# Optimization experiments

Measured on AMD Instinct MI355X. Metric: run time of the kernel, lower is better.

Reference implementation:

```python
import jax, jax.numpy as jnp
import numpy as np

EPS = 1e-5

def _ln(x, g, b):
    m = jnp.mean(x, axis=-1, keepdims=True)
    v = jnp.mean((x - m) ** 2, axis=-1, keepdims=True)
    return (x - m) / jnp.sqrt(v + EPS) * g + b

B, SX, SY = 2, 2048, 2048
XD, YD, P, H, MULT = 1024, 1024, 64, 16, 4

def setup_inputs() -> dict:
    key = jax.random.key(0)
    ks = jax.random.split(key, 20)
    s = lambda fan: 1.0 / np.sqrt(fan)
    return {
        "x": jax.random.normal(ks[0], (B, SX, XD), jnp.float32),
        "y": jax.random.normal(ks[1], (B, SY, YD), jnp.float32),
        "gx_gamma": jnp.ones((XD,), jnp.float32),
        "gx_beta": jnp.zeros((XD,), jnp.float32),
        "gy_gamma": jnp.ones((YD,), jnp.float32),
        "gy_beta": jnp.zeros((YD,), jnp.float32),
        "Wq": jax.random.uniform(ks[2], (H, XD, P), jnp.float32, -s(XD), s(XD)),
        "bq": jax.random.uniform(ks[3], (H, P), jnp.float32, -s(XD), s(XD)),
        "Wk": jax.random.uniform(ks[4], (H, YD, P), jnp.float32, -s(YD), s(YD)),
        "bk": jax.random.uniform(ks[5], (H, P), jnp.float32, -s(YD), s(YD)),
        "Wv": jax.random.uniform(ks[6], (H, YD, P), jnp.float32, -s(YD), s(YD)),
        "bv": jax.random.uniform(ks[7], (H, P), jnp.float32, -s(YD), s(YD)),
        "Wo": jax.random.uniform(ks[8], (H * P, XD), jnp.float32, -s(H * P), s(H * P)),
        "bo": jax.random.uniform(ks[9], (XD,), jnp.float32, -s(H * P), s(H * P)),
        "gd_gamma": jnp.ones((XD,), jnp.float32),
        "gd_beta": jnp.zeros((XD,), jnp.float32),
        "W1": jax.random.uniform(ks[10], (XD, MULT * XD), jnp.float32, -s(XD), s(XD)),
        "b1": jax.random.uniform(ks[11], (MULT * XD,), jnp.float32, -s(XD), s(XD)),
        "W2": jax.random.uniform(ks[12], (MULT * XD, XD), jnp.float32, -s(MULT * XD), s(MULT * XD)),
        "b2": jax.random.uniform(ks[13], (XD,), jnp.float32, -s(MULT * XD), s(MULT * XD)),
        "mask": 1,
    }

def reference(x, y, gx_gamma, gx_beta, gy_gamma, gy_beta, Wq, bq, Wk, bk, Wv, bv,
              Wo, bo, gd_gamma, gd_beta, W1, b1, W2, b2, mask):
    xn = _ln(x, gx_gamma, gx_beta)
    yn = _ln(y, gy_gamma, gy_beta)
    # batched per-head projections: [B,S,D] x [H,D,P] -> [B,H,S,P]
    q = jnp.einsum('bsd,hdp->bhsp', xn, Wq) + bq[None, :, None, :]
    k = jnp.einsum('btd,hdp->bhtp', yn, Wk) + bk[None, :, None, :]
    v = jnp.einsum('btd,hdp->bhtp', yn, Wv) + bv[None, :, None, :]
    scores = jnp.einsum('bhsp,bhtp->bhst', q, k) * (1.0 / jnp.sqrt(jnp.float32(P)))
    attn = jax.nn.softmax(scores, axis=-1)
    if mask:
        # post-softmax strictly-upper-triangular mask (torch.triu diagonal=1)
        tri = jnp.triu(jnp.ones((SX, SY), attn.dtype), k=1)
        attn = attn * tri
    o = jnp.einsum('bhst,bhtp->bhsp', attn, v)          # [B,H,S,P]
    o = o.transpose(0, 2, 1, 3).reshape(B, SX, H * P)    # concat heads
    x2 = x + o @ Wo + bo
    h = jax.nn.gelu(_ln(x2, gd_gamma, gd_beta) @ W1 + b1, approximate=False)
    return x2 + h @ W2 + b2
```

## Files before the change

kernel.cpp:

```cpp
#include <hip/hip_runtime.h>
#include <hip/hip_bf16.h>
#include <math.h>

typedef __bf16 bf16_t;
typedef __bf16 bf16x8 __attribute__((ext_vector_type(8)));
typedef __bf16 bf16x4 __attribute__((ext_vector_type(4)));
typedef float f32x4 __attribute__((ext_vector_type(4)));

#define QSCALE 0.18033688011112042f

static __device__ __forceinline__ f32x4 mfma16(bf16x8 a, bf16x8 b, f32x4 c) {
  return __builtin_amdgcn_mfma_f32_16x16x32_bf16(a, b, c, 0, 0, 0);
}

static __device__ __forceinline__ float exp2_fast(float x) {
  float r;
  asm("v_exp_f32 %0, %1" : "=v"(r) : "v"(x));
  return r;
}

static __device__ __forceinline__ float gelu_f(float x) {
  const float u = x * (0.7978845608028654f + 0.03567740813636141f * x * x);
  const float a = fminf(u * 2.885390081777927f, 126.0f);
  const float e = exp2_fast(a);
  float r;
  asm("v_rcp_f32 %0, %1" : "=v"(r) : "v"(e + 1.0f));
  return x * e * r;
}

typedef __attribute__((address_space(1))) const void as1_void;
typedef __attribute__((address_space(3))) void as3_void;
static __device__ __forceinline__ void gload16(const void* g, void* s) {
  __builtin_amdgcn_global_load_lds((as1_void*)g, (as3_void*)s, 16, 0, 0);
}

static __device__ __forceinline__ long hmi(int row, int col) {
  return ((((long)(row >> 11) * 16 + (col >> 6)) * 2048) + (row & 2047)) * 64 + (col & 63);
}

__global__ __launch_bounds__(256) void prep_all(
    const float* __restrict__ Wq, const float* __restrict__ Wk, const float* __restrict__ Wv,
    const float* __restrict__ Wo, const float* __restrict__ W1, const float* __restrict__ W2,
    bf16_t* __restrict__ WqkvT, bf16_t* __restrict__ WoT, bf16_t* __restrict__ W1T,
    bf16_t* __restrict__ W2T, const float* __restrict__ x, const float* __restrict__ y,
    const float* __restrict__ gx, const float* __restrict__ bex, const float* __restrict__ gy,
    const float* __restrict__ bey, bf16_t* __restrict__ xn, bf16_t* __restrict__ yn) {
  const int bid = blockIdx.x;
  if (bid >= 3072) {
    const int lrow = bid - 3072;
    const float* in = lrow < 4096 ? x : y;
    const float* g = lrow < 4096 ? gx : gy;
    const float* be = lrow < 4096 ? bex : bey;
    bf16_t* out = lrow < 4096 ? xn : yn;
    const int row = lrow & 4095;
    const int t = threadIdx.x;
    const float4 xv = ((const float4*)(in + (long)row * 1024))[t];
    float s1 = xv.x + xv.y + xv.z + xv.w;
    float s2 = xv.x * xv.x + xv.y * xv.y + xv.z * xv.z + xv.w * xv.w;
#pragma unroll
    for (int m = 1; m < 64; m <<= 1) {
      s1 += __shfl_xor(s1, m);
      s2 += __shfl_xor(s2, m);
    }
    __shared__ float r1[4], r2[4];
    if ((t & 63) == 0) { r1[t >> 6] = s1; r2[t >> 6] = s2; }
    __syncthreads();
    s1 = r1[0] + r1[1] + r1[2] + r1[3];
    s2 = r2[0] + r2[1] + r2[2] + r2[3];
    const float mean = s1 * (1.0f / 1024.0f);
    float var = s2 * (1.0f / 1024.0f) - mean * mean;
    const float rstd = rsqrtf(fmaxf(var, 0.0f) + 1e-5f);
    const float4 gv = ((const float4*)g)[t];
    const float4 bv = ((const float4*)be)[t];
    bf16x4 o;
    o[0] = (bf16_t)((xv.x - mean) * rstd * gv.x + bv.x);
    o[1] = (bf16_t)((xv.y - mean) * rstd * gv.y + bv.y);
    o[2] = (bf16_t)((xv.z - mean) * rstd * gv.z + bv.z);
    o[3] = (bf16_t)((xv.w - mean) * rstd * gv.w + bv.w);
    *(bf16x4*)(out + (long)row * 1024 + t * 4) = o;
    return;
  }
  const float* inp;
  bf16_t* outp;
  int istride, ostride, i0, j0;
  if (bid < 768) {
    const int wsel = bid >> 8, rem = bid & 255;
    const int h = rem >> 4, xt = rem & 15;
    const float* W = wsel == 0 ? Wq : (wsel == 1 ? Wk : Wv);
    inp = W + h * 65536;
    outp = WqkvT + (long)wsel * 1048576 + h * 65536;
    istride = 64; ostride = 1024; i0 = xt * 64; j0 = 0;
  } else if (bid < 1024) {
    const int rem = bid - 768;
    inp = Wo; outp = WoT; istride = 1024; ostride = 1024;
    i0 = (rem & 15) * 64; j0 = (rem >> 4) * 64;
  } else if (bid < 2048) {
    const int rem = bid - 1024;
    inp = W1; outp = W1T; istride = 4096; ostride = 1024;
    i0 = (rem & 15) * 64; j0 = (rem >> 4) * 64;
  } else {
    const int rem = bid - 2048;
    inp = W2; outp = W2T; istride = 1024; ostride = 4096;
    i0 = (rem >> 4) * 64; j0 = (rem & 15) * 64;
  }
  __shared__ bf16_t tile[64][65];
  const int r = threadIdx.x >> 2, cs = (threadIdx.x & 3) * 16;
#pragma unroll
  for (int jj = 0; jj < 16; jj++)
    tile[cs + jj][r] = (bf16_t)inp[(long)(i0 + r) * istride + j0 + cs + jj];
  __syncthreads();
#pragma unroll
  for (int jj = 0; jj < 16; jj++)
    outp[(long)(j0 + r) * ostride + i0 + cs + jj] = tile[r][cs + jj];
}

__global__ __launch_bounds__(256) void ln_kernel(const float* __restrict__ in,
                                                 const float* __restrict__ g,
                                                 const float* __restrict__ be,
                                                 bf16_t* __restrict__ out) {
  const int row = blockIdx.x, t = threadIdx.x;
  const float4 xv = ((const float4*)(in + (long)row * 1024))[t];
  float s1 = xv.x + xv.y + xv.z + xv.w;
  float s2 = xv.x * xv.x + xv.y * xv.y + xv.z * xv.z + xv.w * xv.w;
#pragma unroll
  for (int m = 1; m < 64; m <<= 1) {
    s1 += __shfl_xor(s1, m);
    s2 += __shfl_xor(s2, m);
  }
  __shared__ float r1[4], r2[4];
  if ((t & 63) == 0) { r1[t >> 6] = s1; r2[t >> 6] = s2; }
  __syncthreads();
  s1 = r1[0] + r1[1] + r1[2] + r1[3];
  s2 = r2[0] + r2[1] + r2[2] + r2[3];
  const float mean = s1 * (1.0f / 1024.0f);
  float var = s2 * (1.0f / 1024.0f) - mean * mean;
  const float rstd = rsqrtf(fmaxf(var, 0.0f) + 1e-5f);
  const float4 gv = ((const float4*)g)[t];
  const float4 bv = ((const float4*)be)[t];
  bf16x4 o;
  o[0] = (bf16_t)((xv.x - mean) * rstd * gv.x + bv.x);
  o[1] = (bf16_t)((xv.y - mean) * rstd * gv.y + bv.y);
  o[2] = (bf16_t)((xv.z - mean) * rstd * gv.z + bv.z);
  o[3] = (bf16_t)((xv.w - mean) * rstd * gv.w + bv.w);
  *(bf16x4*)(out + (long)row * 1024 + t * 4) = o;
}

__global__ __launch_bounds__(256) void reduce_w2(const bf16_t* __restrict__ part,
                                                 const float* __restrict__ b2,
                                                 float* __restrict__ out) {
  const long base = (long)blockIdx.x * 1024 + threadIdx.x * 4;
  float4 o = *(float4*)(out + base);
  const float4 bb = ((const float4*)b2)[threadIdx.x];
  float s0 = 0.0f, s1 = 0.0f, s2 = 0.0f, s3 = 0.0f;
#pragma unroll
  for (int s = 0; s < 4; s++) {
    bf16x4 p = *(const bf16x4*)(part + ((long)s << 22) + base);
    s0 += (float)p[0];
    s1 += (float)p[1];
    s2 += (float)p[2];
    s3 += (float)p[3];
  }
  o.x += s0 + bb.x;
  o.y += s1 + bb.y;
  o.z += s2 + bb.z;
  o.w += s3 + bb.w;
  *(float4*)(out + base) = o;
}

template <int EPI, int RW>
__global__ __launch_bounds__(512, 2) void gemm256(const bf16_t* __restrict__ A,
                                                  const bf16_t* __restrict__ Bt,
                                                  const float* __restrict__ bias,
                                                  void* __restrict__ Cout,
                                                  int M, int N, int K) {
  __shared__ bf16_t a_l[2][2][256 * 32];
  __shared__ bf16_t b_l[2][2][256 * 32];
  const int tid = threadIdx.x, l = tid & 63, wid = tid >> 6;
  const int wr = wid >> 2, wc = wid & 3;
  const int lr = l & 15, lg = l >> 4;
  const int nwg = gridDim.x * gridDim.y * gridDim.z;
  const int orig = (blockIdx.z * gridDim.y + blockIdx.y) * gridDim.x + blockIdx.x;
  int bx, by, ks = 0;
  if (EPI == 7) {
    const int lid = (orig & 7) * (nwg >> 3) + (orig >> 3);
    bx = lid % gridDim.x;
    by = (lid / gridDim.x) % gridDim.y;
    ks = lid / (gridDim.x * gridDim.y);
  } else {
    const int cpx = nwg >> 3;
    const int xcd = orig & 7, ii = orig >> 3;
    const int rpr = gridDim.x / RW;
    bx = (xcd % rpr) * RW + (ii % RW);
    by = (xcd / rpr) * (cpx / RW) + (ii / RW);
  }
  const int m0 = by * 256, n0 = bx * 256;
  const long kbase = (EPI == 7) ? (long)ks << 10 : 0;
  const int nt = (EPI == 7) ? 16 : (K >> 6);
  const int sr0 = tid >> 2, sr1 = 128 + (tid >> 2);
  const int sch2 = ((tid & 3) ^ ((tid >> 3) & 3)) * 8;
  const int sl0 = sr0 * 32 + (tid & 3) * 8;
  const int sl1 = sr1 * 32 + (tid & 3) * 8;
#define STG_A(bufi, kki, kcol)                                                  \
  do {                                                                          \
    gload16(A + (long)(m0 + sr0) * K + (kcol) + sch2, &a_l[bufi][kki][sl0]);    \
    gload16(A + (long)(m0 + sr1) * K + (kcol) + sch2, &a_l[bufi][kki][sl1]);    \
  } while (0)
#define STG_B(bufi, kki, kcol)                                                  \
  do {                                                                          \
    gload16(Bt + (long)(n0 + sr0) * K + (kcol) + sch2, &b_l[bufi][kki][sl0]);   \
    gload16(Bt + (long)(n0 + sr1) * K + (kcol) + sch2, &b_l[bufi][kki][sl1]);   \
  } while (0)
  const int ch = (lg ^ ((lr >> 1) & 3)) * 8;
  f32x4 acc[8][4] = {};
  bf16x8 af[8], bf2[2];
  STG_A(0, 0, kbase + 0); STG_B(0, 0, kbase + 0);
  STG_A(0, 1, kbase + 32); STG_B(0, 1, kbase + 32);
  STG_A(1, 0, kbase + 64); STG_B(1, 0, kbase + 64);
  asm volatile("s_waitcnt vmcnt(8)" ::: "memory");
  __builtin_amdgcn_s_barrier();
  for (int t = 0; t < nt; t++) {
    const int buf = t & 1, nbuf = buf ^ 1;
    const long kc = kbase + (long)t * 64;
#define RD_A(kki)                                                      \
  _Pragma("unroll") for (int m = 0; m < 8; m++) af[m] =                \
      *(const bf16x8*)&a_l[buf][kki][(wr * 128 + m * 16 + lr) * 32 + ch];
#define RD_B(kki, nh)                                                  \
  _Pragma("unroll") for (int j = 0; j < 2; j++) bf2[j] =               \
      *(const bf16x8*)&b_l[buf][kki][(wc * 64 + ((nh)*2 + j) * 16 + lr) * 32 + ch];
#define MM(nh)                                                         \
  __builtin_amdgcn_s_setprio(1);                                       \
  _Pragma("unroll") for (int m = 0; m < 8; m++) {                      \
    acc[m][(nh)*2 + 0] = mfma16(af[m], bf2[0], acc[m][(nh)*2 + 0]);    \
    acc[m][(nh)*2 + 1] = mfma16(af[m], bf2[1], acc[m][(nh)*2 + 1]);    \
  }                                                                    \
  __builtin_amdgcn_s_setprio(0);
    RD_A(0); RD_B(0, 0);
    if (t + 1 < nt) { STG_A(nbuf, 1, kc + 96); }
    __builtin_amdgcn_s_barrier();
    asm volatile("s_waitcnt lgkmcnt(0)" ::: "memory");
    __builtin_amdgcn_sched_barrier(0);
    MM(0);
    __builtin_amdgcn_s_barrier();
    RD_B(0, 1);
    if (t + 1 < nt) { STG_B(nbuf, 1, kc + 96); }
    if (t + 1 < nt) asm volatile("s_waitcnt vmcnt(8)" ::: "memory");
    else            asm volatile("s_waitcnt vmcnt(0)" ::: "memory");
    __builtin_amdgcn_s_barrier();
    asm volatile("s_waitcnt lgkmcnt(0)" ::: "memory");
    __builtin_amdgcn_sched_barrier(0);
    MM(1);
    __builtin_amdgcn_s_barrier();
    RD_A(1); RD_B(1, 0);
    if (t + 2 < nt) { STG_A(buf, 0, kc + 128); }
    __builtin_amdgcn_s_barrier();
    asm volatile("s_waitcnt lgkmcnt(0)" ::: "memory");
    __builtin_amdgcn_sched_barrier(0);
    MM(0);
    __builtin_amdgcn_s_barrier();
    RD_B(1, 1);
    if (t + 2 < nt) { STG_B(buf, 0, kc + 128); }
    if (t + 2 < nt)      asm volatile("s_waitcnt vmcnt(8)" ::: "memory");
    else if (t + 1 < nt) asm volatile("s_waitcnt vmcnt(4)" ::: "memory");
    __builtin_amdgcn_s_barrier();
    asm volatile("s_waitcnt lgkmcnt(0)" ::: "memory");
    __builtin_amdgcn_sched_barrier(0);
    MM(1);
    __builtin_amdgcn_s_barrier();
  }
#undef RD_A
#undef RD_B
#undef MM
#undef STG_A
#undef STG_B
#pragma unroll
  for (int m = 0; m < 8; m++)
#pragma unroll
    for (int n = 0; n < 4; n++) {
      const int row_b = m0 + wr * 128 + m * 16 + lg * 4;
      const int col = n0 + wc * 64 + n * 16 + lr;
      if (EPI == 2) {
        const float bia = bias[col];
#pragma unroll
        for (int r = 0; r < 4; r++) {
          const long idx = (long)(row_b + r) * N + col;
          ((bf16_t*)Cout)[idx] = (bf16_t)gelu_f(acc[m][n][r] + bia);
        }
      } else if (EPI == 7) {
        bf16_t* part = (bf16_t*)Cout + ((long)ks << 22);
#pragma unroll
        for (int r = 0; r < 4; r++)
          part[(long)(row_b + r) * N + col] = (bf16_t)acc[m][n][r];
      }
    }
}

template <int EPI, int BN, int RW>
__global__ __launch_bounds__(256) void gemm32(const bf16_t* __restrict__ A,
                                              const bf16_t* __restrict__ A2,
                                              const bf16_t* __restrict__ Bt,
                                              const float* __restrict__ bias,
                                              const float* __restrict__ biasB,
                                              const float* __restrict__ biasC,
                                              bf16_t* __restrict__ aux,
                                              void* __restrict__ Cout,
                                              int M, int N, int K) {
  constexpr int NF = BN / 32;
  constexpr int NBI = BN / 64;
  __shared__ bf16_t a_lds[3][128 * 32];
  __shared__ bf16_t b_lds[3][BN * 32];
  const int tid = threadIdx.x, l = tid & 63, w = tid >> 6;
  const int wr = w >> 1, wc = w & 1;
  const int nwg = gridDim.x * gridDim.y;
  const int orig = blockIdx.y * gridDim.x + blockIdx.x;
  const int cpx = nwg >> 3;
  const int xcd = orig & 7, ii = orig >> 3;
  const int rpr = gridDim.x / RW;
  const int bx = (xcd % rpr) * RW + (ii % RW);
  const int by = (xcd / rpr) * (cpx / RW) + (ii / RW);
  const int m0 = by * 128, n0 = bx * BN;
  const bf16_t* Ause = (EPI == 5 && n0 >= 1024) ? A2 : A;
  const int lr = l & 15, lg = l >> 4;
  long a_src[2];
  int a_dst[2];
#pragma unroll
  for (int i = 0; i < 2; i++) {
    const int row = i * 64 + (tid >> 2);
    const int sc = ((tid & 3) ^ ((row >> 1) & 3)) * 8;
    a_src[i] = (long)(m0 + row) * K + sc;
    a_dst[i] = (i * 64 + w * 16) * 32;
  }
  long b_src[NBI];
#pragma unroll
  for (int i = 0; i < NBI; i++) {
    const int row = i * 64 + (tid >> 2);
    const int sc = ((tid & 3) ^ ((row >> 1) & 3)) * 8;
    b_src[i] = (long)(n0 + row) * K + sc;
  }
  const int nk = K >> 5;
  f32x4 acc[4][NF] = {};
#pragma unroll
  for (int tt = 0; tt < 2; tt++) {
#pragma unroll
    for (int i = 0; i < 2; i++) gload16(Ause + a_src[i] + tt * 32, &a_lds[tt][a_dst[i]]);
#pragma unroll
    for (int i = 0; i < NBI; i++) gload16(Bt + b_src[i] + tt * 32, &b_lds[tt][a_dst[i]]);
  }
  int cu = 0;
  for (int t = 0; t < nk; t++) {
    if (t + 1 < nk) asm volatile("s_waitcnt vmcnt(4)" ::: "memory");
    else            asm volatile("s_waitcnt vmcnt(0)" ::: "memory");
    __builtin_amdgcn_s_barrier();
    __builtin_amdgcn_sched_barrier(0);
    if (t + 2 < nk) {
      const long k0 = (long)(t + 2) * 32;
      const int nb = cu >= 1 ? cu - 1 : 2;
#pragma unroll
      for (int i = 0; i < 2; i++) gload16(Ause + a_src[i] + k0, &a_lds[nb][a_dst[i]]);
#pragma unroll
      for (int i = 0; i < NBI; i++) gload16(Bt + b_src[i] + k0, &b_lds[nb][a_dst[i]]);
    }
    const char* ab = (const char*)&a_lds[cu][0];
    const char* bb = (const char*)&b_lds[cu][0];
    bf16x8 af[4], bfr[NF];
#pragma unroll
    for (int m = 0; m < 4; m++) {
      const int row = wr * 64 + m * 16 + lr;
      af[m] = *(const bf16x8*)(ab + row * 64 + 16 * (lg ^ ((row >> 1) & 3)));
    }
#pragma unroll
    for (int n = 0; n < NF; n++) {
      const int row = wc * (BN / 2) + n * 16 + lr;
      bfr[n] = *(const bf16x8*)(bb + row * 64 + 16 * (lg ^ ((row >> 1) & 3)));
    }
    __builtin_amdgcn_s_setprio(1);
#pragma unroll
    for (int m = 0; m < 4; m++)
#pragma unroll
      for (int n = 0; n < NF; n++) acc[m][n] = mfma16(af[m], bfr[n], acc[m][n]);
    __builtin_amdgcn_s_setprio(0);
    cu = cu < 2 ? cu + 1 : 0;
  }
#pragma unroll
  for (int m = 0; m < 4; m++)
#pragma unroll
    for (int n = 0; n < NF; n++) {
      const int row_b = m0 + wr * 64 + m * 16 + (l >> 4) * 4;
      const int col = n0 + wc * (BN / 2) + n * 16 + lr;
      if (EPI == 5) {
        if (col < 1024) {
          const float bia = bias[col];
#pragma unroll
          for (int r = 0; r < 4; r++)
            ((bf16_t*)Cout)[hmi(row_b + r, col)] = (bf16_t)((acc[m][n][r] + bia) * QSCALE);
        } else if (col < 2048) {
          const float bia = biasB[col - 1024];
#pragma unroll
          for (int r = 0; r < 4; r++)
            ((bf16_t*)Cout + 4194304)[hmi(row_b + r, col - 1024)] =
                (bf16_t)(acc[m][n][r] + bia);
        } else {
          const int vcol = col - 2048;
          const float bia = biasC[vcol];
          bf16x4 vv;
#pragma unroll
          for (int r = 0; r < 4; r++) vv[r] = (bf16_t)(acc[m][n][r] + bia);
          const int bb2 = row_b >> 11, tt = row_b & 2047;
          *(bf16x4*)&aux[(((long)(bb2 << 4) + (vcol >> 6)) * 64 + (vcol & 63)) * 2048 + tt] = vv;
        }
      }
    }
}

template <int EPI, int BN>
__global__ __launch_bounds__(256) void gemm64(const bf16_t* __restrict__ A,
                                              const bf16_t* __restrict__ Bt,
                                              const float* __restrict__ bias,
                                              const float* __restrict__ res,
                                              void* __restrict__ Cout,
                                              int M, int N, int K) {
  constexpr int NF = BN / 32;
  constexpr int NBI = BN / 32;
  __shared__ bf16_t a_lds[2][128 * 64];
  __shared__ bf16_t b_lds[2][BN * 64];
  const int tid = threadIdx.x, l = tid & 63, w = tid >> 6;
  const int wr = w >> 1, wc = w & 1;
  const int nwg = gridDim.x * gridDim.y;
  const int orig = blockIdx.y * gridDim.x + blockIdx.x;
  const int lid = (orig & 7) * (nwg >> 3) + (orig >> 3);
  const int bx = lid % gridDim.x, by = lid / gridDim.x;
  const int m0 = by * 128, n0 = bx * BN;
  const int lr = l & 15, lg = l >> 4;
  long a_src[4];
  int ldst[4];
#pragma unroll
  for (int i = 0; i < 4; i++) {
    const int row = i * 32 + w * 8 + (l >> 3);
    const int sc = ((l & 7) ^ (row & 7)) * 8;
    a_src[i] = (long)(m0 + row) * K + sc;
    ldst[i] = (i * 32 + w * 8) * 64;
  }
  long b_src[NBI];
#pragma unroll
  for (int i = 0; i < NBI; i++) {
    const int row = i * 32 + w * 8 + (l >> 3);
    const int sc = ((l & 7) ^ (row & 7)) * 8;
    b_src[i] = (long)(n0 + row) * K + sc;
  }
  const int nk = K >> 6;
  f32x4 acc[4][NF] = {};
#pragma unroll
  for (int i = 0; i < 4; i++) gload16(A + a_src[i], &a_lds[0][ldst[i]]);
#pragma unroll
  for (int i = 0; i < NBI; i++) gload16(Bt + b_src[i], &b_lds[0][ldst[i]]);
  __syncthreads();
  const int sw = (lr & 7) << 4;
  int cur = 0;
  for (int t = 0; t < nk; t++) {
    if (t + 1 < nk) {
      const long k0 = (long)(t + 1) * 64;
#pragma unroll
      for (int i = 0; i < 4; i++) gload16(A + a_src[i] + k0, &a_lds[cur ^ 1][ldst[i]]);
#pragma unroll
      for (int i = 0; i < NBI; i++) gload16(Bt + b_src[i] + k0, &b_lds[cur ^ 1][ldst[i]]);
    }
    const char* ab = (const char*)&a_lds[cur][0];
    const char* bb = (const char*)&b_lds[cur][0];
    bf16x8 af[4][2], bfr[NF][2];
#pragma unroll
    for (int m = 0; m < 4; m++) {
      const int rb = (wr * 64 + m * 16 + lr) * 128;
      af[m][0] = *(const bf16x8*)(ab + rb + ((16 * lg) ^ sw));
      af[m][1] = *(const bf16x8*)(ab + rb + ((16 * lg + 64) ^ sw));
    }
#pragma unroll
    for (int n = 0; n < NF; n++) {
      const int rb = (wc * (BN / 2) + n * 16 + lr) * 128;
      bfr[n][0] = *(const bf16x8*)(bb + rb + ((16 * lg) ^ sw));
      bfr[n][1] = *(const bf16x8*)(bb + rb + ((16 * lg + 64) ^ sw));
    }
    __builtin_amdgcn_s_setprio(1);
#pragma unroll
    for (int kk = 0; kk < 2; kk++)
#pragma unroll
      for (int m = 0; m < 4; m++)
#pragma unroll
        for (int n = 0; n < NF; n++)
          acc[m][n] = mfma16(af[m][kk], bfr[n][kk], acc[m][n]);
    __builtin_amdgcn_s_setprio(0);
    __syncthreads();
    cur ^= 1;
  }
#pragma unroll
  for (int m = 0; m < 4; m++)
#pragma unroll
    for (int n = 0; n < NF; n++) {
      const int row_b = m0 + wr * 64 + m * 16 + (l >> 4) * 4;
      const int col = n0 + wc * (BN / 2) + n * 16 + lr;
      const float bia = bias[col];
#pragma unroll
      for (int r = 0; r < 4; r++) {
        const long idx = (long)(row_b + r) * N + col;
        ((float*)Cout)[idx] = acc[m][n][r] + bia + res[idx];
      }
    }
}

__global__ __launch_bounds__(256) void attn_kernel(const bf16_t* __restrict__ qhm,
                                                   const bf16_t* __restrict__ khm,
                                                   const bf16_t* __restrict__ vtg,
                                                   bf16_t* __restrict__ og,
                                                   const int* __restrict__ maskp) {
  const int T = 2048, HP = 1024;
  __shared__ bf16_t k_lds[2][64 * 64];
  __shared__ bf16_t vt_lds[2][64 * 64];
  __shared__ bf16_t p_lds[4 * 32 * 72];
  const int bh = blockIdx.x, b = bh >> 4, h = bh & 15;
  const int q0 = blockIdx.y * 128;
  const int tid = threadIdx.x, l = tid & 63, w = tid >> 6;
  const int lr = l & 15, lg = l >> 4, lg4 = lg * 4;
  const int srow0 = q0 + w * 32 + lr;
  const bf16_t* kbase = khm + (long)bh * T * 64;
  const bf16_t* vbase = vtg + (long)bh * 64 * T;
  bf16x8 qf[2][2];
#pragma unroll
  for (int g = 0; g < 2; g++) {
    const bf16_t* qr = qhm + ((long)bh * 2048 + srow0 + g * 16) * 64 + lg * 8;
    qf[g][0] = *(const bf16x8*)qr;
    qf[g][1] = *(const bf16x8*)(qr + 32);
  }
  bf16_t* pl = &p_lds[w * 32 * 72];
  float lpart[2] = {0.0f, 0.0f};
  f32x4 oat[4][2] = {};

  const int swz = (lr & 7) << 4;
  const int fo0 = lr * 128 + ((16 * lg) ^ swz);
  const int fo1 = lr * 128 + ((64 + 16 * lg) ^ swz);

  const bool do_mask = (maskp[0] != 0);
  const int nM = do_mask ? (q0 >> 6) : 0;
  const int nt = T >> 6;

  const int sch = l & 7, srow8 = l >> 3;
  int cur = 0;
  {
    const bool needV = (nM == 0);
#pragma unroll
    for (int i = 0; i < 2; i++) {
      const int row = (i * 4 + w) * 8 + srow8;
      const int sc = (sch ^ (row & 7)) * 8;
      gload16(kbase + (long)row * 64 + sc, &k_lds[0][(i * 4 + w) * 512]);
      if (needV) gload16(vbase + (long)row * 2048 + 0 + sc, &vt_lds[0][(i * 4 + w) * 512]);
    }
  }
  __syncthreads();

  for (int t = 0; t < nt; t++) {
    const int t0 = t << 6;
    const int mode = (t < nM) ? 0 : ((do_mask && t < nM + 2) ? 1 : 2);
    if (t + 1 < nt) {
      const int t1 = (t + 1) << 6;
      const bool needV = (t + 1) >= nM;
#pragma unroll
      for (int i = 0; i < 2; i++) {
        const int row = (i * 4 + w) * 8 + srow8;
        const int sc = (sch ^ (row & 7)) * 8;
        gload16(kbase + (long)(t1 + row) * 64 + sc, &k_lds[cur ^ 1][(i * 4 + w) * 512]);
        if (needV)
          gload16(vbase + (long)row * 2048 + t1 + sc, &vt_lds[cur ^ 1][(i * 4 + w) * 512]);
      }
    }
    const char* kb = (const char*)&k_lds[cur][0];
    f32x4 sacc[4][2];
    __builtin_amdgcn_s_setprio(1);
#pragma unroll
    for (int n = 0; n < 4; n++) {
      bf16x8 kf0 = *(const bf16x8*)(kb + n * 2048 + fo0);
      bf16x8 kf1 = *(const bf16x8*)(kb + n * 2048 + fo1);
#pragma unroll
      for (int g = 0; g < 2; g++) {
        f32x4 z = {0.0f, 0.0f, 0.0f, 0.0f};
        z = mfma16(kf0, qf[g][0], z);
        sacc[n][g] = mfma16(kf1, qf[g][1], z);
      }
    }
    __builtin_amdgcn_s_setprio(0);
    float pv[2][4][4];
#pragma unroll
    for (int g = 0; g < 2; g++) {
      float psn[4];
#pragma unroll
      for (int n = 0; n < 4; n++) {
        pv[g][n][0] = exp2_fast(sacc[n][g][0]);
        pv[g][n][1] = exp2_fast(sacc[n][g][1]);
        pv[g][n][2] = exp2_fast(sacc[n][g][2]);
        pv[g][n][3] = exp2_fast(sacc[n][g][3]);
        psn[n] = (pv[g][n][0] + pv[g][n][1]) + (pv[g][n][2] + pv[g][n][3]);
      }
      lpart[g] += (psn[0] + psn[1]) + (psn[2] + psn[3]);
    }
    if (mode > 0) {
#pragma unroll
      for (int g = 0; g < 2; g++)
#pragma unroll
        for (int n = 0; n < 4; n++) {
          bf16x4 pk;
#pragma unroll
          for (int r = 0; r < 4; r++) {
            float v = pv[g][n][r];
            if (mode == 1 && (t0 + n * 16 + lg4 + r) <= srow0 + g * 16) v = 0.0f;
            pk[r] = (bf16_t)v;
          }
          *(bf16x4*)&pl[(g * 16 + lr) * 72 + n * 16 + lg4] = pk;
        }
      const char* vtb = (const char*)&vt_lds[cur][0];
      __builtin_amdgcn_s_setprio(1);
#pragma unroll
      for (int kk = 0; kk < 2; kk++) {
        bf16x8 pb0 = *(bf16x8*)&pl[lr * 72 + kk * 32 + lg * 8];
        bf16x8 pb1 = *(bf16x8*)&pl[(16 + lr) * 72 + kk * 32 + lg * 8];
        const int fkk = lr * 128 + ((kk * 64 + 16 * lg) ^ swz);
#pragma unroll
        for (int np = 0; np < 4; np++) {
          bf16x8 vtf = *(const bf16x8*)(vtb + np * 2048 + fkk);
          oat[np][0] = mfma16(vtf, pb0, oat[np][0]);
          oat[np][1] = mfma16(vtf, pb1, oat[np][1]);
        }
      }
      __builtin_amdgcn_s_setprio(0);
    }
    __syncthreads();
    cur ^= 1;
  }
  float inv[2];
#pragma unroll
  for (int g = 0; g < 2; g++) {
    float lsum = lpart[g];
    lsum += __shfl_xor(lsum, 16);
    lsum += __shfl_xor(lsum, 32);
    inv[g] = 1.0f / lsum;
  }
#pragma unroll
  for (int g = 0; g < 2; g++)
#pragma unroll
    for (int np = 0; np < 4; np++) {
      bf16x4 o4;
#pragma unroll
      for (int r = 0; r < 4; r++) o4[r] = (bf16_t)(oat[np][g][r] * inv[g]);
      *(bf16x4*)&pl[(g * 16 + lr) * 72 + np * 16 + lg4] = o4;
    }
  const int es = l >> 2, ec = (l & 3) * 16;
#pragma unroll
  for (int g = 0; g < 2; g++) {
    bf16x8 o0 = *(bf16x8*)&pl[(g * 16 + es) * 72 + ec];
    bf16x8 o1 = *(bf16x8*)&pl[(g * 16 + es) * 72 + ec + 8];
    bf16_t* orow = og + (long)(b * 2048 + q0 + w * 32 + g * 16 + es) * HP + h * 64 + ec;
    *(bf16x8*)&orow[0] = o0;
    *(bf16x8*)&orow[8] = o1;
  }
}

extern "C" void kernel_launch(void* const* d_in, const int* in_sizes, int n_in,
                              void* d_out, int out_size, void* d_ws, size_t ws_size,
                              hipStream_t stream) {
  const float* x = (const float*)d_in[0];
  const float* y = (const float*)d_in[1];
  const float* gxg = (const float*)d_in[2];
  const float* gxb = (const float*)d_in[3];
  const float* gyg = (const float*)d_in[4];
  const float* gyb = (const float*)d_in[5];
  const float* Wq = (const float*)d_in[6];
  const float* bq = (const float*)d_in[7];
  const float* Wk = (const float*)d_in[8];
  const float* bk = (const float*)d_in[9];
  const float* Wv = (const float*)d_in[10];
  const float* bv = (const float*)d_in[11];
  const float* Wo = (const float*)d_in[12];
  const float* bo = (const float*)d_in[13];
  const float* gdg = (const float*)d_in[14];
  const float* gdb = (const float*)d_in[15];
  const float* W1 = (const float*)d_in[16];
  const float* b1 = (const float*)d_in[17];
  const float* W2 = (const float*)d_in[18];
  const float* b2 = (const float*)d_in[19];
  const int* maskp = (const int*)d_in[20];
  float* out = (float*)d_out;

  char* ws = (char*)d_ws;
  const long MB = 1024 * 1024;
  bf16_t* xn = (bf16_t*)(ws + 0);
  bf16_t* yn = (bf16_t*)(ws + 8 * MB);
  bf16_t* WqkvT = (bf16_t*)(ws + 16 * MB);
  bf16_t* WoT = (bf16_t*)(ws + 22 * MB);
  bf16_t* W1T = (bf16_t*)(ws + 24 * MB);
  bf16_t* W2T = (bf16_t*)(ws + 32 * MB);
  bf16_t* qhm = (bf16_t*)(ws + 40 * MB);
  bf16_t* vTb = (bf16_t*)(ws + 64 * MB);
  bf16_t* ob = (bf16_t*)(ws + 0);
  bf16_t* xd = (bf16_t*)(ws + 8 * MB);
  bf16_t* hb = (bf16_t*)(ws + 40 * MB);
  bf16_t* w2part = (bf16_t*)(ws + 0);
  bf16_t* khm = qhm + 4194304;

  prep_all<<<11264, 256, 0, stream>>>(Wq, Wk, Wv, Wo, W1, W2, WqkvT, WoT, W1T, W2T, x, y, gxg,
                                      gxb, gyg, gyb, xn, yn);
  gemm32<5, 128, 12><<<dim3(24, 32), 256, 0, stream>>>(xn, yn, WqkvT, bq, bk, bv, vTb, qhm,
                                                       4096, 3072, 1024);
  attn_kernel<<<dim3(32, 16), 256, 0, stream>>>(qhm, khm, vTb, ob, maskp);
  gemm64<1, 64><<<dim3(16, 32), 256, 0, stream>>>(ob, WoT, bo, x, out, 4096, 1024, 1024);
  ln_kernel<<<4096, 256, 0, stream>>>(out, gdg, gdb, xd);
  gemm256<2, 4><<<dim3(16, 16), 512, 0, stream>>>(xd, W1T, b1, hb, 4096, 4096, 1024);
  gemm256<7, 4><<<dim3(4, 16, 4), 512, 0, stream>>>(hb, W2T, nullptr, w2part, 4096, 1024, 4096);
  reduce_w2<<<4096, 256, 0, stream>>>(w2part, b2, out);
}
```

Baseline: 224.8 us.

## Split attention over the key dimension into two partitions, then combine

The attention kernel now takes a third grid dimension that splits the 2048 keys into two halves of 16 tiles each. Each half writes an unnormalized bf16 partial output and its partial softmax denominator to workspace. A new attn_combine kernel adds the two partials, divides by the summed denominator and writes the head-concatenated output. The aim is more blocks and better balance across CUs under the triangular mask, at the cost of an extra launch and extra global traffic for the partials.

```diff
diff --git a/kernel.cpp b/kernel.cpp
--- a/kernel.cpp
+++ b/kernel.cpp
@@ -165,6 +165,24 @@
   o.z += s2 + bb.z;
   o.w += s3 + bb.w;
   *(float4*)(out + base) = o;
+}
+
+__global__ __launch_bounds__(256) void attn_combine(const bf16_t* __restrict__ opart,
+                                                    const float* __restrict__ dpart,
+                                                    bf16_t* __restrict__ ob) {
+  const int bid = blockIdx.x, t = threadIdx.x;
+  const int b = bid >> 11, s = bid & 2047;
+  const int col = t * 4, h = col >> 6, p = col & 63;
+  const int bh = b * 16 + h;
+  const float d = dpart[bh * 2048 + s] + dpart[65536 + bh * 2048 + s];
+  const float inv = 1.0f / d;
+  const long pbase = ((long)bh * 2048 + s) * 64 + p;
+  bf16x4 p0 = *(const bf16x4*)(opart + pbase);
+  bf16x4 p1 = *(const bf16x4*)(opart + 4194304 + pbase);
+  bf16x4 o;
+#pragma unroll
+  for (int r = 0; r < 4; r++) o[r] = (bf16_t)(((float)p0[r] + (float)p1[r]) * inv);
+  *(bf16x4*)(ob + (long)bid * 1024 + col) = o;
 }
 
 template <int EPI, int RW>
@@ -508,14 +526,17 @@
 __global__ __launch_bounds__(256) void attn_kernel(const bf16_t* __restrict__ qhm,
                                                    const bf16_t* __restrict__ khm,
                                                    const bf16_t* __restrict__ vtg,
-                                                   bf16_t* __restrict__ og,
+                                                   bf16_t* __restrict__ opart,
+                                                   float* __restrict__ dpart,
                                                    const int* __restrict__ maskp) {
-  const int T = 2048, HP = 1024;
+  const int T = 2048;
   __shared__ bf16_t k_lds[2][64 * 64];
   __shared__ bf16_t vt_lds[2][64 * 64];
   __shared__ bf16_t p_lds[4 * 32 * 72];
-  const int bh = blockIdx.x, b = bh >> 4, h = bh & 15;
+  const int bh = blockIdx.x;
   const int q0 = blockIdx.y * 128;
+  const int z = blockIdx.z;
+  const int tg0 = z * 16;
   const int tid = threadIdx.x, l = tid & 63, w = tid >> 6;
   const int lr = l & 15, lg = l >> 4, lg4 = lg * 4;
   const int srow0 = q0 + w * 32 + lr;
@@ -538,28 +559,29 @@
 
   const bool do_mask = (maskp[0] != 0);
   const int nM = do_mask ? (q0 >> 6) : 0;
-  const int nt = T >> 6;
 
   const int sch = l & 7, srow8 = l >> 3;
   int cur = 0;
   {
-    const bool needV = (nM == 0);
+    const int t0 = tg0 << 6;
+    const bool needV = (tg0 >= nM);
 #pragma unroll
     for (int i = 0; i < 2; i++) {
       const int row = (i * 4 + w) * 8 + srow8;
       const int sc = (sch ^ (row & 7)) * 8;
-      gload16(kbase + (long)row * 64 + sc, &k_lds[0][(i * 4 + w) * 512]);
-      if (needV) gload16(vbase + (long)row * 2048 + 0 + sc, &vt_lds[0][(i * 4 + w) * 512]);
+      gload16(kbase + (long)(t0 + row) * 64 + sc, &k_lds[0][(i * 4 + w) * 512]);
+      if (needV) gload16(vbase + (long)row * 2048 + t0 + sc, &vt_lds[0][(i * 4 + w) * 512]);
     }
   }
   __syncthreads();
 
-  for (int t = 0; t < nt; t++) {
-    const int t0 = t << 6;
-    const int mode = (t < nM) ? 0 : ((do_mask && t < nM + 2) ? 1 : 2);
-    if (t + 1 < nt) {
-      const int t1 = (t + 1) << 6;
-      const bool needV = (t + 1) >= nM;
+  for (int tl = 0; tl < 16; tl++) {
+    const int tg = tg0 + tl;
+    const int t0 = tg << 6;
+    const int mode = (tg < nM) ? 0 : ((do_mask && tg < nM + 2) ? 1 : 2);
+    if (tl + 1 < 16) {
+      const int t1 = (tg + 1) << 6;
+      const bool needV = (tg + 1) >= nM;
 #pragma unroll
       for (int i = 0; i < 2; i++) {
         const int row = (i * 4 + w) * 8 + srow8;
@@ -578,9 +600,9 @@
       bf16x8 kf1 = *(const bf16x8*)(kb + n * 2048 + fo1);
 #pragma unroll
       for (int g = 0; g < 2; g++) {
-        f32x4 z = {0.0f, 0.0f, 0.0f, 0.0f};
-        z = mfma16(kf0, qf[g][0], z);
-        sacc[n][g] = mfma16(kf1, qf[g][1], z);
+        f32x4 zz = {0.0f, 0.0f, 0.0f, 0.0f};
+        zz = mfma16(kf0, qf[g][0], zz);
+        sacc[n][g] = mfma16(kf1, qf[g][1], zz);
       }
     }
     __builtin_amdgcn_s_setprio(0);
@@ -631,13 +653,13 @@
     __syncthreads();
     cur ^= 1;
   }
-  float inv[2];
 #pragma unroll
   for (int g = 0; g < 2; g++) {
     float lsum = lpart[g];
     lsum += __shfl_xor(lsum, 16);
     lsum += __shfl_xor(lsum, 32);
-    inv[g] = 1.0f / lsum;
+    if (lg == 0)
+      dpart[z * 65536 + bh * 2048 + q0 + w * 32 + g * 16 + lr] = lsum;
   }
 #pragma unroll
   for (int g = 0; g < 2; g++)
@@ -645,15 +667,16 @@
     for (int np = 0; np < 4; np++) {
       bf16x4 o4;
 #pragma unroll
-      for (int r = 0; r < 4; r++) o4[r] = (bf16_t)(oat[np][g][r] * inv[g]);
+      for (int r = 0; r < 4; r++) o4[r] = (bf16_t)oat[np][g][r];
       *(bf16x4*)&pl[(g * 16 + lr) * 72 + np * 16 + lg4] = o4;
     }
   const int es = l >> 2, ec = (l & 3) * 16;
+  bf16_t* obase = opart + (long)z * 4194304;
 #pragma unroll
   for (int g = 0; g < 2; g++) {
     bf16x8 o0 = *(bf16x8*)&pl[(g * 16 + es) * 72 + ec];
     bf16x8 o1 = *(bf16x8*)&pl[(g * 16 + es) * 72 + ec + 8];
-    bf16_t* orow = og + (long)(b * 2048 + q0 + w * 32 + g * 16 + es) * HP + h * 64 + ec;
+    bf16_t* orow = obase + ((long)bh * 2048 + q0 + w * 32 + g * 16 + es) * 64 + ec;
     *(bf16x8*)&orow[0] = o0;
     *(bf16x8*)&orow[8] = o1;
   }
@@ -695,7 +718,9 @@
   bf16_t* W2T = (bf16_t*)(ws + 32 * MB);
   bf16_t* qhm = (bf16_t*)(ws + 40 * MB);
   bf16_t* vTb = (bf16_t*)(ws + 64 * MB);
-  bf16_t* ob = (bf16_t*)(ws + 0);
+  bf16_t* opart = (bf16_t*)(ws + 0);
+  float* dpart = (float*)(ws + 16 * MB);
+  bf16_t* ob = (bf16_t*)(ws + 56 * MB);
   bf16_t* xd = (bf16_t*)(ws + 8 * MB);
   bf16_t* hb = (bf16_t*)(ws + 40 * MB);
   bf16_t* w2part = (bf16_t*)(ws + 0);
@@ -705,7 +730,8 @@
                                       gxb, gyg, gyb, xn, yn);
   gemm32<5, 128, 12><<<dim3(24, 32), 256, 0, stream>>>(xn, yn, WqkvT, bq, bk, bv, vTb, qhm,
                                                        4096, 3072, 1024);
-  attn_kernel<<<dim3(32, 16), 256, 0, stream>>>(qhm, khm, vTb, ob, maskp);
+  attn_kernel<<<dim3(32, 16, 2), 256, 0, stream>>>(qhm, khm, vTb, opart, dpart, maskp);
+  attn_combine<<<4096, 256, 0, stream>>>(opart, dpart, ob);
   gemm64<1, 64><<<dim3(16, 32), 256, 0, stream>>>(ob, WoT, bo, x, out, 4096, 1024, 1024);
   ln_kernel<<<4096, 256, 0, stream>>>(out, gdg, gdb, xd);
   gemm256<2, 4><<<dim3(16, 16), 512, 0, stream>>>(xd, W1T, b1, hb, 4096, 4096, 1024);
```

New measurement: 233.4 us. 1.04x slower.

## Split attention block across eight waves with sixteen query rows each

Applied to the files above, without the earlier changes.

The attention kernel now launches 512 threads per block instead of 256, so each of eight waves owns 16 query rows rather than 32. Per-wave register state (Q fragments, score and output accumulators) is halved, and each thread loads one K/V chunk per tile instead of two. The aim is more waves in flight to hide LDS and exp latency. The cost is less reuse of each K/V fragment read from LDS across query rows, plus more waves contending at each block barrier.

```diff
diff --git a/kernel.cpp b/kernel.cpp
--- a/kernel.cpp
+++ b/kernel.cpp
@@ -505,7 +505,7 @@
     }
 }
 
-__global__ __launch_bounds__(256) void attn_kernel(const bf16_t* __restrict__ qhm,
+__global__ __launch_bounds__(512) void attn_kernel(const bf16_t* __restrict__ qhm,
                                                    const bf16_t* __restrict__ khm,
                                                    const bf16_t* __restrict__ vtg,
                                                    bf16_t* __restrict__ og,
@@ -513,24 +513,20 @@
   const int T = 2048, HP = 1024;
   __shared__ bf16_t k_lds[2][64 * 64];
   __shared__ bf16_t vt_lds[2][64 * 64];
-  __shared__ bf16_t p_lds[4 * 32 * 72];
+  __shared__ bf16_t p_lds[8 * 16 * 72];
   const int bh = blockIdx.x, b = bh >> 4, h = bh & 15;
   const int q0 = blockIdx.y * 128;
   const int tid = threadIdx.x, l = tid & 63, w = tid >> 6;
   const int lr = l & 15, lg = l >> 4, lg4 = lg * 4;
-  const int srow0 = q0 + w * 32 + lr;
+  const int srow = q0 + w * 16 + lr;
   const bf16_t* kbase = khm + (long)bh * T * 64;
   const bf16_t* vbase = vtg + (long)bh * 64 * T;
-  bf16x8 qf[2][2];
-#pragma unroll
-  for (int g = 0; g < 2; g++) {
-    const bf16_t* qr = qhm + ((long)bh * 2048 + srow0 + g * 16) * 64 + lg * 8;
-    qf[g][0] = *(const bf16x8*)qr;
-    qf[g][1] = *(const bf16x8*)(qr + 32);
-  }
-  bf16_t* pl = &p_lds[w * 32 * 72];
-  float lpart[2] = {0.0f, 0.0f};
-  f32x4 oat[4][2] = {};
+  const bf16_t* qr = qhm + ((long)bh * 2048 + srow) * 64 + lg * 8;
+  bf16x8 qf0 = *(const bf16x8*)qr;
+  bf16x8 qf1 = *(const bf16x8*)(qr + 32);
+  bf16_t* pl = &p_lds[w * 16 * 72];
+  float lpart = 0.0f;
+  f32x4 oat[4] = {};
 
   const int swz = (lr & 7) << 4;
   const int fo0 = lr * 128 + ((16 * lg) ^ swz);
@@ -540,17 +536,14 @@
   const int nM = do_mask ? (q0 >> 6) : 0;
   const int nt = T >> 6;
 
-  const int sch = l & 7, srow8 = l >> 3;
+  const int srow8 = l >> 3, sch = l & 7;
+  const int ssc = (sch ^ srow8) * 8;
+  const int srw = w * 8 + srow8;
   int cur = 0;
   {
     const bool needV = (nM == 0);
-#pragma unroll
-    for (int i = 0; i < 2; i++) {
-      const int row = (i * 4 + w) * 8 + srow8;
-      const int sc = (sch ^ (row & 7)) * 8;
-      gload16(kbase + (long)row * 64 + sc, &k_lds[0][(i * 4 + w) * 512]);
-      if (needV) gload16(vbase + (long)row * 2048 + 0 + sc, &vt_lds[0][(i * 4 + w) * 512]);
-    }
+    gload16(kbase + (long)srw * 64 + ssc, &k_lds[0][w * 512]);
+    if (needV) gload16(vbase + (long)srw * 2048 + 0 + ssc, &vt_lds[0][w * 512]);
   }
   __syncthreads();
 
@@ -560,70 +553,53 @@
     if (t + 1 < nt) {
       const int t1 = (t + 1) << 6;
       const bool needV = (t + 1) >= nM;
-#pragma unroll
-      for (int i = 0; i < 2; i++) {
-        const int row = (i * 4 + w) * 8 + srow8;
-        const int sc = (sch ^ (row & 7)) * 8;
-        gload16(kbase + (long)(t1 + row) * 64 + sc, &k_lds[cur ^ 1][(i * 4 + w) * 512]);
-        if (needV)
-          gload16(vbase + (long)row * 2048 + t1 + sc, &vt_lds[cur ^ 1][(i * 4 + w) * 512]);
-      }
+      gload16(kbase + (long)(t1 + srw) * 64 + ssc, &k_lds[cur ^ 1][w * 512]);
+      if (needV) gload16(vbase + (long)srw * 2048 + t1 + ssc, &vt_lds[cur ^ 1][w * 512]);
     }
     const char* kb = (const char*)&k_lds[cur][0];
-    f32x4 sacc[4][2];
+    f32x4 sacc[4];
     __builtin_amdgcn_s_setprio(1);
 #pragma unroll
     for (int n = 0; n < 4; n++) {
       bf16x8 kf0 = *(const bf16x8*)(kb + n * 2048 + fo0);
       bf16x8 kf1 = *(const bf16x8*)(kb + n * 2048 + fo1);
-#pragma unroll
-      for (int g = 0; g < 2; g++) {
-        f32x4 z = {0.0f, 0.0f, 0.0f, 0.0f};
-        z = mfma16(kf0, qf[g][0], z);
-        sacc[n][g] = mfma16(kf1, qf[g][1], z);
+      f32x4 z = {0.0f, 0.0f, 0.0f, 0.0f};
+      z = mfma16(kf0, qf0, z);
+      sacc[n] = mfma16(kf1, qf1, z);
+    }
+    __builtin_amdgcn_s_setprio(0);
+    float pv[4][4], psn[4];
+#pragma unroll
+    for (int n = 0; n < 4; n++) {
+      pv[n][0] = exp2_fast(sacc[n][0]);
+      pv[n][1] = exp2_fast(sacc[n][1]);
+      pv[n][2] = exp2_fast(sacc[n][2]);
+      pv[n][3] = exp2_fast(sacc[n][3]);
+      psn[n] = (pv[n][0] + pv[n][1]) + (pv[n][2] + pv[n][3]);
+    }
+    lpart += (psn[0] + psn[1]) + (psn[2] + psn[3]);
+    if (mode > 0) {
+#pragma unroll
+      for (int n = 0; n < 4; n++) {
+        bf16x4 pk;
+#pragma unroll
+        for (int r = 0; r < 4; r++) {
+          float v = pv[n][r];
+          if (mode == 1 && (t0 + n * 16 + lg4 + r) <= srow) v = 0.0f;
+          pk[r] = (bf16_t)v;
+        }
+        *(bf16x4*)&pl[lr * 72 + n * 16 + lg4] = pk;
       }
-    }
-    __builtin_amdgcn_s_setprio(0);
-    float pv[2][4][4];
-#pragma unroll
-    for (int g = 0; g < 2; g++) {
-      float psn[4];
-#pragma unroll
-      for (int n = 0; n < 4; n++) {
-        pv[g][n][0] = exp2_fast(sacc[n][g][0]);
-        pv[g][n][1] = exp2_fast(sacc[n][g][1]);
-        pv[g][n][2] = exp2_fast(sacc[n][g][2]);
-        pv[g][n][3] = exp2_fast(sacc[n][g][3]);
-        psn[n] = (pv[g][n][0] + pv[g][n][1]) + (pv[g][n][2] + pv[g][n][3]);
-      }
-      lpart[g] += (psn[0] + psn[1]) + (psn[2] + psn[3]);
-    }
-    if (mode > 0) {
-#pragma unroll
-      for (int g = 0; g < 2; g++)
-#pragma unroll
-        for (int n = 0; n < 4; n++) {
-          bf16x4 pk;
-#pragma unroll
-          for (int r = 0; r < 4; r++) {
-            float v = pv[g][n][r];
-            if (mode == 1 && (t0 + n * 16 + lg4 + r) <= srow0 + g * 16) v = 0.0f;
-            pk[r] = (bf16_t)v;
-          }
-          *(bf16x4*)&pl[(g * 16 + lr) * 72 + n * 16 + lg4] = pk;
-        }
       const char* vtb = (const char*)&vt_lds[cur][0];
       __builtin_amdgcn_s_setprio(1);
 #pragma unroll
       for (int kk = 0; kk < 2; kk++) {
-        bf16x8 pb0 = *(bf16x8*)&pl[lr * 72 + kk * 32 + lg * 8];
-        bf16x8 pb1 = *(bf16x8*)&pl[(16 + lr) * 72 + kk * 32 + lg * 8];
+        bf16x8 pb = *(bf16x8*)&pl[lr * 72 + kk * 32 + lg * 8];
         const int fkk = lr * 128 + ((kk * 64 + 16 * lg) ^ swz);
 #pragma unroll
         for (int np = 0; np < 4; np++) {
           bf16x8 vtf = *(const bf16x8*)(vtb + np * 2048 + fkk);
-          oat[np][0] = mfma16(vtf, pb0, oat[np][0]);
-          oat[np][1] = mfma16(vtf, pb1, oat[np][1]);
+          oat[np] = mfma16(vtf, pb, oat[np]);
         }
       }
       __builtin_amdgcn_s_setprio(0);
@@ -631,32 +607,23 @@
     __syncthreads();
     cur ^= 1;
   }
-  float inv[2];
-#pragma unroll
-  for (int g = 0; g < 2; g++) {
-    float lsum = lpart[g];
-    lsum += __shfl_xor(lsum, 16);
-    lsum += __shfl_xor(lsum, 32);
-    inv[g] = 1.0f / lsum;
-  }
-#pragma unroll
-  for (int g = 0; g < 2; g++)
-#pragma unroll
-    for (int np = 0; np < 4; np++) {
-      bf16x4 o4;
-#pragma unroll
-      for (int r = 0; r < 4; r++) o4[r] = (bf16_t)(oat[np][g][r] * inv[g]);
-      *(bf16x4*)&pl[(g * 16 + lr) * 72 + np * 16 + lg4] = o4;
-    }
+  float lsum = lpart;
+  lsum += __shfl_xor(lsum, 16);
+  lsum += __shfl_xor(lsum, 32);
+  const float inv = 1.0f / lsum;
+#pragma unroll
+  for (int np = 0; np < 4; np++) {
+    bf16x4 o4;
+#pragma unroll
+    for (int r = 0; r < 4; r++) o4[r] = (bf16_t)(oat[np][r] * inv);
+    *(bf16x4*)&pl[lr * 72 + np * 16 + lg4] = o4;
+  }
   const int es = l >> 2, ec = (l & 3) * 16;
-#pragma unroll
-  for (int g = 0; g < 2; g++) {
-    bf16x8 o0 = *(bf16x8*)&pl[(g * 16 + es) * 72 + ec];
-    bf16x8 o1 = *(bf16x8*)&pl[(g * 16 + es) * 72 + ec + 8];
-    bf16_t* orow = og + (long)(b * 2048 + q0 + w * 32 + g * 16 + es) * HP + h * 64 + ec;
-    *(bf16x8*)&orow[0] = o0;
-    *(bf16x8*)&orow[8] = o1;
-  }
+  bf16x8 o0 = *(bf16x8*)&pl[es * 72 + ec];
+  bf16x8 o1 = *(bf16x8*)&pl[es * 72 + ec + 8];
+  bf16_t* orow = og + (long)(b * 2048 + q0 + w * 16 + es) * HP + h * 64 + ec;
+  *(bf16x8*)&orow[0] = o0;
+  *(bf16x8*)&orow[8] = o1;
 }
 
 extern "C" void kernel_launch(void* const* d_in, const int* in_sizes, int n_in,
@@ -705,7 +672,7 @@
                                       gxb, gyg, gyb, xn, yn);
   gemm32<5, 128, 12><<<dim3(24, 32), 256, 0, stream>>>(xn, yn, WqkvT, bq, bk, bv, vTb, qhm,
                                                        4096, 3072, 1024);
-  attn_kernel<<<dim3(32, 16), 256, 0, stream>>>(qhm, khm, vTb, ob, maskp);
+  attn_kernel<<<dim3(32, 16), 512, 0, stream>>>(qhm, khm, vTb, ob, maskp);
   gemm64<1, 64><<<dim3(16, 32), 256, 0, stream>>>(ob, WoT, bo, x, out, 4096, 1024, 1024);
   ln_kernel<<<4096, 256, 0, stream>>>(out, gdg, gdb, xd);
   gemm256<2, 4><<<dim3(16, 16), 512, 0, stream>>>(xd, W1T, b1, hb, 4096, 4096, 1024);
```

Result: no change. 220.5 us (median of 2 runs) (-1.9%).
